# Optimization experiments

Hardware: AMD Instinct MI355X
Metric: run time of the kernel (lower is better)

Reference implementation:

```python
import jax, jax.numpy as jnp
import numpy as np

E = 256; D = 512; A = 5; NS = 2048; NQ = 8192; NWAY = 5
_OTHERS = np.array([[j for j in range(A) if j != i] for i in range(A)])  # [A, A-1] indices of other agents
_ROWS = np.arange(A)[:, None]


def _ln(x, g, b, eps=1e-5):
    m = x.mean(-1, keepdims=True)
    v = ((x - m) ** 2).mean(-1, keepdims=True)
    return (x - m) * jax.lax.rsqrt(v + eps) * g + b


def _mha(x, in_w, in_b, out_w, out_b, h, mask=None):
    # torch nn.MultiheadAttention (batch_first) self-attention. in_w: [3E,E], out_w: [E,E]
    B, S, Em = x.shape
    hd = Em // h
    qkv = x @ in_w.T + in_b
    q, k, v = jnp.split(qkv, 3, axis=-1)
    q = q.reshape(B, S, h, hd).transpose(0, 2, 1, 3) * (1.0 / np.sqrt(hd))
    k = k.reshape(B, S, h, hd).transpose(0, 2, 1, 3)
    v = v.reshape(B, S, h, hd).transpose(0, 2, 1, 3)
    s = jnp.einsum('bhqd,bhkd->bhqk', q, k)
    if mask is not None:
        s = jnp.where(mask, s, jnp.asarray(-1e9, s.dtype))
    a = jax.nn.softmax(s, axis=-1)
    o = jnp.einsum('bhqk,bhkd->bhqd', a, v).transpose(0, 2, 1, 3).reshape(B, S, Em)
    return o @ out_w.T + out_b


def _forward(support_x, support_y, query_x, n_way, fe0_w1, fe0_b1, fe0_g1, fe0_be1, fe0_w2, fe0_b2, fe0_g2, fe0_be2, fe1_w1, fe1_b1, fe1_g, fe1_be, fe1_w2, fe1_b2, fe2_w1, fe2_b1, fe2_w2, fe2_b2, fe2_g, fe2_be, fe3_w1, fe3_b1, fe3_w2, fe3_b2, fe3_g, fe3_be, fe4_w1, fe4_b1, fe4_w2, fe4_b2, fe4_w3, fe4_b3, msg_enc_w, msg_enc_b, agg_in_w, agg_in_b, agg_out_w, agg_out_b, proc_w1, proc_b1, proc_w2, proc_b2, internal_state, proto_in_w, proto_in_b, proto_out_w, proto_out_b, cls_w1, cls_b1, cls_w2, cls_b2, cls_w3, cls_b3, comm_w, f_w1, f_b1, f_w2, f_b2, f_w3, f_b3):
    # --- per-agent-type feature extractors (eval mode: dropout off) ---
    def fe0(x):
        h = jax.nn.relu(_ln(x @ fe0_w1 + fe0_b1, fe0_g1, fe0_be1))
        return jax.nn.relu(_ln(h @ fe0_w2 + fe0_b2, fe0_g2, fe0_be2))
    def fe1(x):
        h = jax.nn.relu(_ln(x @ fe1_w1 + fe1_b1, fe1_g, fe1_be))
        return jnp.tanh(h @ fe1_w2 + fe1_b2)
    def fe2(x):
        h = jax.nn.relu(x @ fe2_w1 + fe2_b1)
        return jax.nn.relu(_ln(h @ fe2_w2 + fe2_b2, fe2_g, fe2_be))
    def fe3(x):
        h = jax.nn.relu(x @ fe3_w1 + fe3_b1)
        return jax.nn.sigmoid(_ln(h @ fe3_w2 + fe3_b2, fe3_g, fe3_be))
    def fe4(x):
        h = jax.nn.relu(x @ fe4_w1 + fe4_b1)
        h = jax.nn.relu(h @ fe4_w2 + fe4_b2)
        return h @ fe4_w3 + fe4_b3
    feats_s = jnp.stack([fe0(support_x), fe1(support_x), fe2(support_x), fe3(support_x), fe4(support_x)])  # [A,NS,E]
    feats_q = jnp.stack([fe0(query_x), fe1(query_x), fe2(query_x), fe3(query_x), fe4(query_x)])            # [A,NQ,E]

    # --- one communication round: generate -> weight -> MHA-aggregate -> MLP-process ---
    agent_state = feats_s.mean(1) + internal_state                                         # [A,E]
    messages = jnp.tanh(jnp.einsum('ae,aef->af', agent_state, msg_enc_w) + msg_enc_b)      # [A,E]
    wgt = jax.nn.softmax(comm_w, axis=-1)                                                  # [A,A]
    msgs = messages[_OTHERS] * wgt[_ROWS, _OTHERS][..., None]                              # [A,A-1,E]
    def agg_one(m, iw, ib, ow, ob):
        return _mha(m[None], iw, ib, ow, ob, 4)[0].mean(0)
    agg = jax.vmap(agg_one)(msgs, agg_in_w, agg_in_b, agg_out_w, agg_out_b)                # [A,E]
    comb = internal_state + agg
    hh = jax.nn.relu(jnp.einsum('ae,aef->af', comb, proc_w1) + proc_b1)
    ck = jnp.einsum('ae,aef->af', hh, proc_w2) + proc_b2                                   # [A,E] communicated knowledge

    # --- class-masked prototype attention (equivalent to per-class MHA) + logits ---
    mask = support_y[:, None] == support_y[None, :]                                        # [NS,NS]
    counts = jax.ops.segment_sum(jnp.ones(support_y.shape, jnp.float32), support_y, num_segments=n_way)
    def head(fs, fq, cki, piw, pib, pw, pb, c1, c1b, c2, c2b, c3, c3b):
        att = _mha((fs + cki[None])[None], piw, pib, pw, pb, 2, mask[None, None])[0]       # [NS,E]
        psum = jax.ops.segment_sum(att, support_y, num_segments=n_way)
        protos = jnp.where(counts[:, None] > 0, psum / jnp.maximum(counts, 1.0)[:, None], 0.0)  # [n_way,E]
        eq = jnp.concatenate([fq, jnp.broadcast_to(cki, fq.shape)], axis=-1)               # [NQ,2E]
        d2 = (fq * fq).sum(-1, keepdims=True) + (protos * protos).sum(-1)[None, :] - 2.0 * (fq @ protos.T)
        dist = jnp.sqrt(jnp.maximum(d2, 1e-12))                                            # cdist
        c = jax.nn.relu(eq @ c1 + c1b)
        c = jax.nn.relu(c @ c2 + c2b)
        conf = c @ c3 + c3b                                                                # [NQ,1]
        return -dist + conf * 0.1
    logits = jax.vmap(head)(feats_s, feats_q, ck, proto_in_w, proto_in_b, proto_out_w, proto_out_b, cls_w1, cls_b1, cls_w2, cls_b2, cls_w3, cls_b3)  # [A,NQ,n_way]

    # --- decision fusion over concatenated per-agent query features ---
    qcat = feats_q.transpose(1, 0, 2).reshape(NQ, A * E)
    fh = jax.nn.relu(qcat @ f_w1 + f_b1)
    fh = jax.nn.relu(fh @ f_w2 + f_b2)
    fused = fh @ f_w3 + f_b3                                                               # [NQ,1]
    return logits, fused


def setup_inputs() -> dict:
    key = jax.random.key(0)
    ks = iter(jax.random.split(key, 80))
    def rn(shape, scale=1.0):
        return (jax.random.normal(next(ks), shape) * scale).astype(jnp.float32)
    def lin(shape, fan):
        return rn(shape, 1.0 / np.sqrt(fan))
    z = lambda s: jnp.zeros(s, jnp.float32)
    o = lambda s: jnp.ones(s, jnp.float32)
    inp = {}
    inp['support_x'] = rn((NS, D))
    inp['support_y'] = jax.random.randint(next(ks), (NS,), 0, NWAY, dtype=jnp.int32)
    inp['query_x'] = rn((NQ, D))
    inp['n_way'] = NWAY
    inp['fe0_w1'] = lin((D, 2 * E), D); inp['fe0_b1'] = z((2 * E,)); inp['fe0_g1'] = o((2 * E,)); inp['fe0_be1'] = z((2 * E,))
    inp['fe0_w2'] = lin((2 * E, E), 2 * E); inp['fe0_b2'] = z((E,)); inp['fe0_g2'] = o((E,)); inp['fe0_be2'] = z((E,))
    inp['fe1_w1'] = lin((D, E), D); inp['fe1_b1'] = z((E,)); inp['fe1_g'] = o((E,)); inp['fe1_be'] = z((E,))
    inp['fe1_w2'] = lin((E, E), E); inp['fe1_b2'] = z((E,))
    inp['fe2_w1'] = lin((D, 3 * E), D); inp['fe2_b1'] = z((3 * E,))
    inp['fe2_w2'] = lin((3 * E, E), 3 * E); inp['fe2_b2'] = z((E,)); inp['fe2_g'] = o((E,)); inp['fe2_be'] = z((E,))
    inp['fe3_w1'] = lin((D, E), D); inp['fe3_b1'] = z((E,))
    inp['fe3_w2'] = lin((E, E), E); inp['fe3_b2'] = z((E,)); inp['fe3_g'] = o((E,)); inp['fe3_be'] = z((E,))
    inp['fe4_w1'] = lin((D, 2 * E), D); inp['fe4_b1'] = z((2 * E,))
    inp['fe4_w2'] = lin((2 * E, E), 2 * E); inp['fe4_b2'] = z((E,))
    inp['fe4_w3'] = lin((E, E), E); inp['fe4_b3'] = z((E,))
    inp['msg_enc_w'] = lin((A, E, E), E); inp['msg_enc_b'] = z((A, E))
    inp['agg_in_w'] = lin((A, 3 * E, E), E); inp['agg_in_b'] = z((A, 3 * E))
    inp['agg_out_w'] = lin((A, E, E), E); inp['agg_out_b'] = z((A, E))
    inp['proc_w1'] = lin((A, E, E), E); inp['proc_b1'] = z((A, E))
    inp['proc_w2'] = lin((A, E, E), E); inp['proc_b2'] = z((A, E))
    inp['internal_state'] = rn((A, E), 0.01)
    inp['proto_in_w'] = lin((A, 3 * E, E), E); inp['proto_in_b'] = z((A, 3 * E))
    inp['proto_out_w'] = lin((A, E, E), E); inp['proto_out_b'] = z((A, E))
    inp['cls_w1'] = lin((A, 2 * E, E), 2 * E); inp['cls_b1'] = z((A, E))
    inp['cls_w2'] = lin((A, E, E // 2), E); inp['cls_b2'] = z((A, E // 2))
    inp['cls_w3'] = lin((A, E // 2, 1), E // 2); inp['cls_b3'] = z((A, 1))
    inp['comm_w'] = (jnp.eye(A) * 0.5 + 0.1).astype(jnp.float32)
    inp['f_w1'] = lin((A * E, E), A * E); inp['f_b1'] = z((E,))
    inp['f_w2'] = lin((E, E // 2), E); inp['f_b2'] = z((E // 2,))
    inp['f_w3'] = lin((E // 2, 1), E // 2); inp['f_b3'] = z((1,))
    return inp


def reference(support_x, support_y, query_x, n_way, fe0_w1, fe0_b1, fe0_g1, fe0_be1, fe0_w2, fe0_b2, fe0_g2, fe0_be2, fe1_w1, fe1_b1, fe1_g, fe1_be, fe1_w2, fe1_b2, fe2_w1, fe2_b1, fe2_w2, fe2_b2, fe2_g, fe2_be, fe3_w1, fe3_b1, fe3_w2, fe3_b2, fe3_g, fe3_be, fe4_w1, fe4_b1, fe4_w2, fe4_b2, fe4_w3, fe4_b3, msg_enc_w, msg_enc_b, agg_in_w, agg_in_b, agg_out_w, agg_out_b, proc_w1, proc_b1, proc_w2, proc_b2, internal_state, proto_in_w, proto_in_b, proto_out_w, proto_out_b, cls_w1, cls_b1, cls_w2, cls_b2, cls_w3, cls_b3, comm_w, f_w1, f_b1, f_w2, f_b2, f_w3, f_b3):
    return _forward(support_x, support_y, query_x, n_way, fe0_w1, fe0_b1, fe0_g1, fe0_be1, fe0_w2, fe0_b2, fe0_g2, fe0_be2, fe1_w1, fe1_b1, fe1_g, fe1_be, fe1_w2, fe1_b2, fe2_w1, fe2_b1, fe2_w2, fe2_b2, fe2_g, fe2_be, fe3_w1, fe3_b1, fe3_w2, fe3_b2, fe3_g, fe3_be, fe4_w1, fe4_b1, fe4_w2, fe4_b2, fe4_w3, fe4_b3, msg_enc_w, msg_enc_b, agg_in_w, agg_in_b, agg_out_w, agg_out_b, proc_w1, proc_b1, proc_w2, proc_b2, internal_state, proto_in_w, proto_in_b, proto_out_w, proto_out_b, cls_w1, cls_b1, cls_w2, cls_b2, cls_w3, cls_b3, comm_w, f_w1, f_b1, f_w2, f_b2, f_w3, f_b3)
```

## Files before the change

kernel.cpp:

```cpp
#include <hip/hip_runtime.h>
#include <hip/hip_bf16.h>

typedef __hip_bfloat16 bf16;
typedef short s8v __attribute__((ext_vector_type(8)));
typedef short s4v __attribute__((ext_vector_type(4)));
typedef float f4v __attribute__((ext_vector_type(4)));

#define A_  5
#define D_  512
#define E_  256
#define NS_ 2048
#define NQ_ 8192
#define NM_ 10240
#define NWAY_ 5
#define QSCALE 0.088388347648318447f
#define FSTR ((size_t)NM_ * E_)

__device__ inline float ldw(const void* p, size_t i, int f32) {
  return f32 ? ((const float*)p)[i] : __bfloat162float(((const bf16*)p)[i]);
}
template<bool DYN>
__device__ inline float ldT(const void* p, size_t i, int f32) {
  if (DYN) return ldw(p, i, f32);
  return ((const float*)p)[i];
}

__device__ inline short f2bf(float v) {
  union { float f; unsigned u; } x; x.f = v;
  unsigned r = x.u + 0x7fffu + ((x.u >> 16) & 1u);
  return (short)(r >> 16);
}
__device__ inline float bf2f(short s) {
  union { unsigned u; float f; } x; x.u = ((unsigned)(unsigned short)s) << 16;
  return x.f;
}

__device__ __forceinline__ void gload16(const void* g, void* l) {
  __builtin_amdgcn_global_load_lds(
      (const __attribute__((address_space(1))) unsigned int*)g,
      (__attribute__((address_space(3))) unsigned int*)l, 16, 0, 0);
}

struct Ptrs { const void* p[64]; int sz[64]; };

__global__ void probe_k(Ptrs P, int* flags) {
  int b = blockIdx.x, lane = threadIdx.x;
  if (b == 1 || b == 3) { if (lane == 0) flags[b] = 0; return; }
  const bf16* t = (const bf16*)P.p[b];
  int n = P.sz[b];
  int K = (n >> 1) < 64 ? (n >> 1) : 64;
  bool big = false, eNZ = false, oNZ = false;
  if (lane < K) {
    float e = __bfloat162float(t[2 * lane]);
    float o = __bfloat162float(t[2 * lane + 1]);
    big = !(fabsf(e) <= 1e3f);
    eNZ = (e != 0.f); oNZ = (o != 0.f);
  }
  unsigned long long bb = __ballot(big), eb = __ballot(eNZ), ob = __ballot(oNZ);
  if (lane == 0) flags[b] = (bb != 0ull || (eb == 0ull && ob != 0ull)) ? 1 : 0;
}

__global__ void classidx_k(const int* __restrict__ y, int* __restrict__ idx,
                           int* __restrict__ cnt, int* __restrict__ cstart) {
  __shared__ int sc[NWAY_];
  int tid = threadIdx.x;
  if (tid < NWAY_) sc[tid] = 0;
  __syncthreads();
  for (int i = tid; i < NS_; i += 256) {
    int c = y[i];
    int pos = atomicAdd(&sc[c], 1);
    idx[c * NS_ + pos] = i;
  }
  __syncthreads();
  if (tid < NWAY_) cnt[tid] = sc[tid];
  if (tid == 0) { int s = 0; for (int q = 0; q < NWAY_; ++q) { cstart[q] = s; s += sc[q]; } }
}

__global__ void xcopy_k(const void* __restrict__ sx, const void* __restrict__ qx,
                        short* __restrict__ XC, const int* __restrict__ flags) {
  size_t i = ((size_t)blockIdx.x * 256 + threadIdx.x) * 4;
  const size_t SN = (size_t)NS_ * 512;
  if (i < SN) {
    int f = flags[0];
    #pragma unroll
    for (int q = 0; q < 4; ++q) XC[i + q] = f2bf(ldw(sx, i + q, f));
  } else {
    int f = flags[2];
    size_t j = i - SN;
    #pragma unroll
    for (int q = 0; q < 4; ++q) XC[i + q] = f2bf(ldw(qx, j + q, f));
  }
}

__global__ void wcat_k(Ptrs P, short* __restrict__ Wcat, float* __restrict__ bcat,
                       const int* __restrict__ flags) {
  int n = blockIdx.x * 256 + threadIdx.x;
  int k = blockIdx.y;
  int iw, ib, nl, Nloc;
  if (n < 512)       { iw = 4;  ib = 5;  nl = n;        Nloc = 512; }
  else if (n < 768)  { iw = 12; ib = 13; nl = n - 512;  Nloc = 256; }
  else if (n < 1536) { iw = 18; ib = 19; nl = n - 768;  Nloc = 768; }
  else if (n < 1792) { iw = 24; ib = 25; nl = n - 1536; Nloc = 256; }
  else               { iw = 30; ib = 31; nl = n - 1792; Nloc = 512; }
  Wcat[(size_t)n * 512 + k] = f2bf(ldw(P.p[iw], (size_t)k * Nloc + nl, flags[iw]));
  if (k == 0) bcat[n] = ldw(P.p[ib], nl, flags[ib]);
}

__global__ void wcls_k(const void* __restrict__ cw1, const void* __restrict__ fw1,
                       short* __restrict__ B2, const int* __restrict__ flags) {
  int n = blockIdx.x, a = blockIdx.y, k = threadIdx.x;
  float v;
  if (n < 256) v = ldw(cw1, ((size_t)a * 512 + k) * 256 + n, flags[51]);
  else v = ldw(fw1, ((size_t)(a * 256 + k)) * 256 + (n - 256), flags[58]);
  B2[((size_t)a * 512 + n) * 256 + k] = f2bf(v);
}

#define LSTR 40
template<int AMODE, int BMODE, bool DYNBIAS, bool TRB, int ACT, bool ACCUM,
         bool KSPLIT = false, bool OUTBF16 = false, bool DOMAP = false>
__global__ __launch_bounds__(256) void gemm_k(
    const void* __restrict__ A, int lda,
    const void* __restrict__ B, int ldb, size_t offB,
    const void* __restrict__ bias, size_t offBias,
    float* __restrict__ C, int ldc,
    int M, int N, int K, float alpha,
    int ia, int ib, int ibias, const int* __restrict__ flags,
    size_t sA, size_t sB, size_t sBias, size_t sC, size_t kstrideA,
    unsigned long long amap)
{
  constexpr bool GDB = (AMODE == 2) && (BMODE == 2) && TRB && !KSPLIT;
  const int fA = (AMODE == 1) ? flags[ia] : 1;
  const int fB = (BMODE == 1) ? flags[ib] : 1;
  const int fBi = DYNBIAS ? flags[ibias] : 1;
  const size_t zA = (size_t)blockIdx.z * sA;
  const size_t zB = offB + (size_t)blockIdx.z * sB;
  const size_t zBias = offBias + (size_t)blockIdx.z * sBias;
  float* Cz = C + (size_t)blockIdx.z * sC;
  bf16* Cz16 = (bf16*)C + (size_t)blockIdx.z * sC;
  const int tid = threadIdx.x;
  const int bm = blockIdx.y * 128, bn = blockIdx.x * 128;
  const int lane = tid & 63, wid = tid >> 6;
  const int lm = lane & 15, quad = lane >> 4;
  const int wy = (wid >> 1) * 64, wx = (wid & 1) * 64;
  f4v acc[4][4];
  #pragma unroll
  for (int i = 0; i < 4; ++i)
    #pragma unroll
    for (int j = 0; j < 4; ++j) acc[i][j] = (f4v)(0.f);

  if constexpr (GDB) {
    __shared__ short smem[4 * 128 * 32];
    const int srow = lane >> 2, scol = (lane & 3) * 8;
    const short* Azs = (const short*)A + zA;
    const short* Bzs = (const short*)B + zB;
    auto stage = [&](int bsel, int k0) {
      short* Asb = smem + bsel * 4096;
      short* Bsb = smem + 8192 + bsel * 4096;
      #pragma unroll
      for (int q = 0; q < 2; ++q) {
        int rb = (wid * 2 + q) * 16;
        gload16(Azs + (size_t)(bm + rb + srow) * lda + k0 + scol, Asb + rb * 32);
        gload16(Bzs + (size_t)(bn + rb + srow) * ldb + k0 + scol, Bsb + rb * 32);
      }
    };
    stage(0, 0);
    __syncthreads();
    int cur = 0;
    for (int k0 = 0; k0 < K; k0 += 32) {
      if (k0 + 32 < K) stage(cur ^ 1, k0 + 32);
      const short* Asb = smem + cur * 4096;
      const short* Bsb = smem + 8192 + cur * 4096;
      s8v af[4], bfr[4];
      #pragma unroll
      for (int mi = 0; mi < 4; ++mi)
        af[mi] = *(const s8v*)&Asb[(wy + mi*16 + lm) * 32 + quad * 8];
      #pragma unroll
      for (int ni = 0; ni < 4; ++ni)
        bfr[ni] = *(const s8v*)&Bsb[(wx + ni*16 + lm) * 32 + quad * 8];
      #pragma unroll
      for (int mi = 0; mi < 4; ++mi)
        #pragma unroll
        for (int ni = 0; ni < 4; ++ni)
          acc[mi][ni] = __builtin_amdgcn_mfma_f32_16x16x32_bf16(af[mi], bfr[ni], acc[mi][ni], 0, 0, 0);
      __syncthreads();
      cur ^= 1;
    }
  } else {
    __shared__ short As[128 * LSTR];
    __shared__ short Bs[128 * LSTR];
    const int am = tid >> 1, ah = (tid & 1) * 16;

    s8v a_s0, a_s1;
    float a_f[16];
    s8v b_s0, b_s1;
    float b_f[16];
    short b_h[16];

    auto loadA = [&](int k0) {
      int kk = k0 + ah;
      size_t base;
      if (KSPLIT) base = zA + (size_t)(kk >> 8) * kstrideA + (size_t)(bm + am) * lda + (kk & 255);
      else base = zA + (size_t)(bm + am) * lda + kk;
      if constexpr (AMODE == 2) {
        const bf16* ap = (const bf16*)A + base;
        a_s0 = *(const s8v*)ap;
        a_s1 = *(const s8v*)(ap + 8);
      } else {
        if (fA) {
          const float4* src = (const float4*)((const float*)A + base);
          #pragma unroll
          for (int q = 0; q < 4; ++q) {
            float4 v = src[q];
            a_f[q*4] = v.x; a_f[q*4+1] = v.y; a_f[q*4+2] = v.z; a_f[q*4+3] = v.w;
          }
        } else {
          #pragma unroll
          for (int q = 0; q < 16; ++q) a_f[q] = ldw(A, base + q, 0);
        }
      }
    };
    auto storeA = [&]() {
      if constexpr (AMODE == 2) {
        *(s8v*)&As[am * LSTR + ah] = a_s0;
        *(s8v*)&As[am * LSTR + ah + 8] = a_s1;
      } else {
        short tmp[16];
        #pragma unroll
        for (int q = 0; q < 16; ++q) tmp[q] = f2bf(a_f[q]);
        s4v* dst = (s4v*)&As[am * LSTR + ah];
        #pragma unroll
        for (int q = 0; q < 4; ++q) dst[q] = *(s4v*)&tmp[q*4];
      }
    };
    auto loadB = [&](int k0) {
      if constexpr (TRB) {
        int n = tid >> 1, h = (tid & 1) * 16;
        size_t base = zB + (size_t)(bn + n) * ldb + k0 + h;
        if constexpr (BMODE == 2) {
          const bf16* bp = (const bf16*)B + base;
          b_s0 = *(const s8v*)bp;
          b_s1 = *(const s8v*)(bp + 8);
        } else {
          if (fB) {
            const float4* src = (const float4*)((const float*)B + base);
            #pragma unroll
            for (int q = 0; q < 4; ++q) {
              float4 v = src[q];
              b_f[q*4] = v.x; b_f[q*4+1] = v.y; b_f[q*4+2] = v.z; b_f[q*4+3] = v.w;
            }
          } else {
            #pragma unroll
            for (int q = 0; q < 16; ++q) b_f[q] = ldw(B, base + q, 0);
          }
        }
      } else {
        int n = tid & 127, kk2 = (tid >> 7) * 16;
        #pragma unroll
        for (int j = 0; j < 16; ++j) {
          size_t bi = zB + (size_t)(k0 + kk2 + j) * ldb + bn + n;
          if constexpr (BMODE == 2) b_h[j] = ((const short*)B)[bi];
          else b_f[j] = ldT<BMODE == 1>(B, bi, fB);
        }
      }
    };
    auto storeB = [&]() {
      if constexpr (TRB) {
        int n = tid >> 1, h = (tid & 1) * 16;
// ... 343 lines not shown
        m_run[ri] = mn;
      }
    }
  }
  if (lm == 0) {
    #pragma unroll
    for (int mi = 0; mi < 4; ++mi)
      #pragma unroll
      for (int r = 0; r < 4; ++r) {
        int row = mi * 16 + quad * 4 + r;
        Mw[wid][row] = m_run[mi * 4 + r];
        Lw[wid][row] = l_run[mi * 4 + r];
      }
  }
  __syncthreads();
  if (tid < 64 && r0 + tid < n) {
    float m = fmaxf(fmaxf(Mw[0][tid], Mw[1][tid]), fmaxf(Mw[2][tid], Mw[3][tid]));
    float l = Lw[0][tid] * __expf(Mw[0][tid] - m) + Lw[1][tid] * __expf(Mw[1][tid] - m)
            + Lw[2][tid] * __expf(Mw[2][tid] - m) + Lw[3][tid] * __expf(Mw[3][tid] - m);
    size_t p = (size_t)z * NS_ + cstart[c] + r0 + tid;
    ml[p * 2] = m; ml[p * 2 + 1] = l;
  }
}

__global__ __launch_bounds__(256) void attn_colsum_k(
    const short* __restrict__ qkv_all, const int* __restrict__ idx,
    const int* __restrict__ cnt, const int* __restrict__ cstart,
    const float* __restrict__ ml, float* __restrict__ colsum)
{
  int c = blockIdx.x, z = blockIdx.z, a = z >> 1, h = z & 1;
  int n = cnt[c];
  int j0 = blockIdx.y * 64;
  if (j0 >= n) return;
  const short* qkv = qkv_all + (size_t)a * NS_ * 768;
  const int* myidx = idx + c * NS_;
  __shared__ short Qs[64 * LS];
  __shared__ short Ks[64 * LS];
  __shared__ float Msm[64], Lsm[64];
  int tid = threadIdx.x, lane = tid & 63, wid = tid >> 6;
  int lm = lane & 15, quad = lane >> 4;
  stage64x128(qkv, myidx, j0, n, 256 + h * 128, Ks);
  float ca = 0.f;
  for (int i0 = 0; i0 < n; i0 += 64) {
    __syncthreads();
    stage64x128(qkv, myidx, i0, n, h * 128, Qs);
    if (tid < 64) {
      int gi = i0 + tid;
      if (gi < n) {
        size_t p = (size_t)z * NS_ + cstart[c] + gi;
        Msm[tid] = ml[p * 2]; Lsm[tid] = ml[p * 2 + 1];
      } else { Msm[tid] = 0.f; Lsm[tid] = 1.f; }
    }
    __syncthreads();
    f4v acc[4];
    #pragma unroll
    for (int mi = 0; mi < 4; ++mi) acc[mi] = (f4v)(0.f);
    #pragma unroll
    for (int kc = 0; kc < 4; ++kc) {
      s8v bfr = *(const s8v*)&Ks[(wid * 16 + lm) * LS + kc * 32 + quad * 8];
      #pragma unroll
      for (int mi = 0; mi < 4; ++mi) {
        s8v af = *(const s8v*)&Qs[(mi * 16 + lm) * LS + kc * 32 + quad * 8];
        acc[mi] = __builtin_amdgcn_mfma_f32_16x16x32_bf16(af, bfr, acc[mi], 0, 0, 0);
      }
    }
    #pragma unroll
    for (int mi = 0; mi < 4; ++mi) {
      #pragma unroll
      for (int r = 0; r < 4; ++r) {
        int lrow = mi * 16 + quad * 4 + r;
        int gi = i0 + lrow;
        if (gi < n) {
          float m = Msm[lrow];
          float invl = 1.f / Lsm[lrow];
          ca += __expf(acc[mi][r] * QSCALE - m) * invl;
        }
      }
    }
  }
  ca += __shfl_xor(ca, 16);
  ca += __shfl_xor(ca, 32);
  int col = j0 + wid * 16 + lm;
  if (quad == 0 && col < n)
    colsum[(size_t)z * NS_ + cstart[c] + col] = ca;
}

#define PCH 8
__global__ __launch_bounds__(1024) void proto_reduce_k(
    const short* __restrict__ qkv_all, const int* __restrict__ idx,
    const int* __restrict__ cnt, const int* __restrict__ cstart,
    const float* __restrict__ colsum, float* __restrict__ proto_pre) {
  int c = blockIdx.x, a = blockIdx.y;
  int n = cnt[c];
  int tid = threadIdx.x, lane = tid & 63, wid = tid >> 6;
  int h = lane >> 5;
  int e0 = lane * 4;
  const short* qkv = qkv_all + (size_t)a * NS_ * 768 + 512;
  const float* csum = colsum + (size_t)(a * 2 + h) * NS_ + cstart[c];
  const int* myidx = idx + c * NS_;
  float a0 = 0.f, a1 = 0.f, a2 = 0.f, a3 = 0.f;
  for (int k = wid; k < n; k += 16) {
    float w = csum[k];
    const s4v v = *(const s4v*)(qkv + (size_t)myidx[k] * 768 + e0);
    a0 += w * bf2f(v[0]); a1 += w * bf2f(v[1]);
    a2 += w * bf2f(v[2]); a3 += w * bf2f(v[3]);
  }
  __shared__ float red[16][E_];
  *(float4*)&red[wid][e0] = make_float4(a0, a1, a2, a3);
  __syncthreads();
  if (tid < E_) {
    float s = 0.f;
    #pragma unroll
    for (int wdx = 0; wdx < 16; ++wdx) s += red[wdx][tid];
    proto_pre[((size_t)a * NWAY_ + c) * E_ + tid] = (n > 0) ? s / (float)n : 0.f;
  }
}

__global__ void proto_outproj_k(const float* __restrict__ proto_pre, const void* __restrict__ ow,
                                const void* __restrict__ ob, const int* __restrict__ cnt,
                                float* __restrict__ protos_all, float* __restrict__ pnorm,
                                const int* __restrict__ flags) {
  int c = blockIdx.x, a = blockIdx.y, e = threadIdx.x;
  const int fW = flags[49], fB = flags[50];
  __shared__ float pp[E_];
  __shared__ float r2[E_];
  pp[e] = proto_pre[((size_t)a * NWAY_ + c) * E_ + e];
  __syncthreads();
  size_t wb = (size_t)a * E_ * E_ + (size_t)e * E_;
  float s = 0.f;
  for (int k = 0; k < E_; ++k) s += pp[k] * ldw(ow, wb + k, fW);
  float v = s + ldw(ob, (size_t)a * E_ + e, fB);
  float vm = (cnt[c] > 0) ? v : 0.f;
  protos_all[((size_t)a * NWAY_ + c) * E_ + e] = vm;
  r2[e] = vm * vm;
  __syncthreads();
  for (int o = 128; o > 0; o >>= 1) { if (e < o) r2[e] += r2[e + o]; __syncthreads(); }
  if (e == 0) pnorm[a * NWAY_ + c] = r2[0];
}

__global__ void bias2_k(const float* __restrict__ ck, const void* __restrict__ w1,
                        const void* __restrict__ b1, float* __restrict__ biascat2,
                        const int* __restrict__ flags) {
  const int fW = flags[51], fB = flags[52];
  int a = blockIdx.x, n = threadIdx.x;
  __shared__ float c[E_];
  c[n] = ck[a * E_ + n]; __syncthreads();
  size_t wbase = (size_t)a * 2 * E_ * E_ + (size_t)E_ * E_ + n;
  float s = 0.f;
  for (int k = 0; k < E_; ++k) s += c[k] * ldw(w1, wbase + (size_t)k * E_, fW);
  biascat2[(size_t)a * 512 + n] = s + ldw(b1, (size_t)a * E_ + n, fB);
  biascat2[(size_t)a * 512 + 256 + n] = 0.f;
}

__global__ void fcomb_k(const short* __restrict__ U, const void* __restrict__ b1,
                        short* __restrict__ fh1, const int* __restrict__ flags) {
  int i = blockIdx.x, n = threadIdx.x;
  const int fB = flags[59];
  float s = 0.f;
  #pragma unroll
  for (int a = 0; a < A_; ++a)
    s += bf2f(U[((size_t)a * NQ_ + i) * 512 + 256 + n]);
  s += ldw(b1, n, fB);
  fh1[(size_t)i * 256 + n] = f2bf(fmaxf(s, 0.f));
}

__global__ __launch_bounds__(64) void logits_k(const short* __restrict__ fqbase,
                                               const float* __restrict__ protos_all,
                                               const float* __restrict__ pnorm,
                                               const bf16* __restrict__ c2all,
                                               const void* __restrict__ w3,
                                               const void* __restrict__ b3,
                                               float* __restrict__ out,
                                               const int* __restrict__ flags) {
  const int fW = flags[55], fB = flags[56];
  int i = blockIdx.x, a = blockIdx.y, lane = threadIdx.x;
  const short* fq = fqbase + (size_t)a * FSTR + (size_t)i * E_ + lane * 4;
  const float* protos = protos_all + (size_t)a * NWAY_ * E_;
  const bf16* c2 = c2all + ((size_t)a * NQ_ + i) * 128;
  s4v xv4 = *(const s4v*)fq;
  float x0 = bf2f(xv4[0]), x1 = bf2f(xv4[1]), x2 = bf2f(xv4[2]), x3 = bf2f(xv4[3]);
  float qq = wave_sum64(x0 * x0 + x1 * x1 + x2 * x2 + x3 * x3);
  float cpart = __bfloat162float(c2[lane * 2]) * ldw(w3, (size_t)a * 128 + lane * 2, fW) +
                __bfloat162float(c2[lane * 2 + 1]) * ldw(w3, (size_t)a * 128 + lane * 2 + 1, fW);
  float conf = wave_sum64(cpart);
  if (lane == 0) conf += ldw(b3, a, fB);
  for (int c = 0; c < NWAY_; ++c) {
    float4 pv = ((const float4*)(protos + c * E_))[lane];
    float dt = wave_sum64(x0 * pv.x + x1 * pv.y + x2 * pv.z + x3 * pv.w);
    if (lane == 0) {
      float pp = pnorm[a * NWAY_ + c];
      float d2 = fmaxf(qq + pp - 2.f * dt, 1e-12f);
      out[((size_t)a * NQ_ + i) * NWAY_ + c] = -sqrtf(d2) + 0.1f * conf;
    }
  }
}

__global__ __launch_bounds__(64) void fused_k(const float* __restrict__ h2, const void* __restrict__ w3,
                                              const void* __restrict__ b3, float* __restrict__ out,
                                              const int* __restrict__ flags) {
  const int fW = flags[62], fB = flags[63];
  int i = blockIdx.x, lane = threadIdx.x;
  float s = h2[(size_t)i * 128 + lane * 2] * ldw(w3, lane * 2, fW) +
            h2[(size_t)i * 128 + lane * 2 + 1] * ldw(w3, lane * 2 + 1, fW);
  s = wave_sum64(s);
  if (lane == 0) out[i] = s + ldw(b3, 0, fB);
}

extern "C" void kernel_launch(void* const* d_in, const int* in_sizes, int n_in,
                              void* d_out, int out_size, void* d_ws, size_t ws_size,
                              hipStream_t stream) {
  (void)out_size; (void)ws_size;
  #define P(i) ((const void*)d_in[i])
  const int* support_y = (const int*)d_in[1];
  float* out = (float*)d_out;

  int* flags = (int*)d_ws;
  char* base = (char*)d_ws + 256;
  short* featsC = (short*)base;
  char* R = base + (size_t)A_ * FSTR * 2;
  short* t1cat   = (short*)R;
  short* qkv_all = (short*)R;
  short* U       = (short*)(R + (size_t)15728640);
  short* fh1     = (short*)R;
  float* fh2     = (float*)(R + (size_t)8388608);
  char* XCR = R + (size_t)57671680;
  short* XC   = (short*)XCR;
  short* tmp2 = (short*)XCR;
  short* b4   = (short*)(XCR + (size_t)NM_ * 256 * 2);
  short* clsC2_all = (short*)XCR;
  char* S = XCR + (size_t)10485760;
  float* state      = (float*)S;
  float* msg        = state + A_ * E_;
  float* ck         = msg + A_ * E_;
  float* protos_all = ck + A_ * E_;
  float* biascat2   = protos_all + A_ * NWAY_ * E_;
  float* ml         = biascat2 + A_ * 512;
  float* colsum     = ml + (size_t)A_ * 2 * NS_ * 2;
  float* proto_pre  = colsum + (size_t)A_ * 2 * NS_;
  int*   idx        = (int*)(proto_pre + A_ * NWAY_ * E_);
  int*   cnt        = idx + NWAY_ * NS_;
  int*   cstart     = cnt + NWAY_;
  float* statepart  = (float*)(cstart + NWAY_ + 3);
  float* mvp        = statepart + A_ * 16 * E_;
  float* qkvc       = mvp + A_ * 8 * E_;
  float* obar       = qkvc + A_ * 4 * 768;
  float* comb       = obar + A_ * E_;
  float* hh         = comb + A_ * E_;
  float* ckb        = hh + A_ * E_;
  float* ppart      = ckb + A_ * 768;
  float* bcat       = ppart + (size_t)A_ * NWAY_ * PCH * E_;
  short* Wcat       = (short*)(bcat + 2304);
  short* Bcat2      = Wcat + (size_t)2304 * 512;

  const short* fq_base = featsC + (size_t)NS_ * E_;

  Ptrs ps;
  for (int i = 0; i < 64; ++i) {
    ps.p[i] = (i < n_in) ? d_in[i] : nullptr;
    ps.sz[i] = (i < n_in) ? in_sizes[i] : 0;
  }
  probe_k<<<64, 64, 0, stream>>>(ps, flags);
  classidx_k<<<1, 256, 0, stream>>>(support_y, idx, cnt, cstart);
  xcopy_k<<<(NM_ * 512 / 4) / 256, 256, 0, stream>>>(P(0), P(2), XC, flags);
  wcat_k<<<dim3(9, 512), 256, 0, stream>>>(ps, Wcat, bcat, flags);
  wcls_k<<<dim3(512, A_), 256, 0, stream>>>(P(51), P(58), Bcat2, flags);

  gemm<2, 2, false, true, 0, false, false, true, true>(
      stream, XC, 512, Wcat, 512, 0, bcat, 0, (float*)t1cat, 2304,
      NM_, 2304, 512, 1.f, -1, -1, -1, flags, 1, 0, 0, 0, 0, 0, 0x555555000ULL);
  lnv_k<1, 512><<<NM_ / 4, 256, 0, stream>>>(t1cat, P(6), P(7), t1cat, 2304, 2304, 6, 7, flags);
  gemm<2, 1, true, false, 0, false, false, true>(stream, t1cat, 2304, P(8), 256, 0, P(9), 0,
                                                 (float*)tmp2, 256, NM_, 256, 512, 1.f, -1, 8, 9, flags);
  lnv_k<1, 256><<<NM_ / 4, 256, 0, stream>>>(tmp2, P(10), P(11), featsC, 256, 256, 10, 11, flags);
  lnv_k<1, 256><<<NM_ / 4, 256, 0, stream>>>(t1cat + 512, P(14), P(15), t1cat + 512, 2304, 2304, 14, 15, flags);
  gemm<2, 1, true, false, 2, false, false, true>(stream, t1cat + 512, 2304, P(16), 256, 0, P(17), 0,
                                                 (float*)(featsC + FSTR), 256, NM_, 256, 256, 1.f, -1, 16, 17, flags);
  gemm<2, 1, true, false, 0, false, false, true>(stream, t1cat + 768, 2304, P(20), 256, 0, P(21), 0,
                                                 (float*)tmp2, 256, NM_, 256, 768, 1.f, -1, 20, 21, flags);
  lnv_k<1, 256><<<NM_ / 4, 256, 0, stream>>>(tmp2, P(22), P(23), featsC + 2 * FSTR, 256, 256, 22, 23, flags);
  gemm<2, 1, true, false, 0, false, false, true>(stream, t1cat + 1536, 2304, P(26), 256, 0, P(27), 0,
                                                 (float*)tmp2, 256, NM_, 256, 256, 1.f, -1, 26, 27, flags);
  lnv_k<3, 256><<<NM_ / 4, 256, 0, stream>>>(tmp2, P(28), P(29), featsC + 3 * FSTR, 256, 256, 28, 29, flags);
  gemm<2, 1, true, false, 1, false, false, true>(stream, t1cat + 1792, 2304, P(32), 256, 0, P(33), 0,
                                                 (float*)b4, 256, NM_, 256, 512, 1.f, -1, 32, 33, flags);
  gemm<2, 1, true, false, 0, false, false, true>(stream, b4, 256, P(34), 256, 0, P(35), 0,
                                                 (float*)(featsC + 4 * FSTR), 256, NM_, 256, 256, 1.f, -1, 34, 35, flags);

  statepart_k<<<dim3(A_, 16), 256, 0, stream>>>(featsC, statepart);
  statecomb_k<<<A_, 256, 0, stream>>>(statepart, P(46), state, flags);
  mvpart_k<<<dim3(A_, 8), 256, 0, stream>>>(state, P(36), 36, mvp, flags);
  mvcomb_k<2><<<A_, 256, 0, stream>>>(mvp, P(37), 37, msg, flags);
  qkvcomm_k<<<A_ * 768 / 4, 256, 0, stream>>>(msg, P(57), P(38), P(39), qkvc, flags);
  attn4_k<<<A_, 256, 0, stream>>>(qkvc, obar);
  combproj_k<<<A_ * E_ / 4, 256, 0, stream>>>(obar, P(40), P(41), P(46), comb, flags);
  mvpart_k<<<dim3(A_, 8), 256, 0, stream>>>(comb, P(42), 42, mvp, flags);
  mvcomb_k<1><<<A_, 256, 0, stream>>>(mvp, P(43), 43, hh, flags);
  mvpart_k<<<dim3(A_, 8), 256, 0, stream>>>(hh, P(44), 44, mvp, flags);
  mvcomb_k<0><<<A_, 256, 0, stream>>>(mvp, P(45), 45, ck, flags);

  ckb_k<<<A_ * 768 / 4, 256, 0, stream>>>(ck, P(47), P(48), ckb, flags);
  gemm<2, 1, false, true, 0, false, false, true>(stream, featsC, 256, P(47), 256, 0, ckb, 0,
                                    (float*)qkv_all, 768, NS_, 768, 256, 1.f, -1, 47, -1, flags,
                                    A_, FSTR, (size_t)3 * E_ * E_, (size_t)768, (size_t)NS_ * 768);
  {
    dim3 g(NWAY_, NS_ / 64, A_ * 2);
    attn_stats_k<<<g, 256, 0, stream>>>(qkv_all, idx, cnt, cstart, ml);
    attn_colsum_k<<<g, 256, 0, stream>>>(qkv_all, idx, cnt, cstart, ml, colsum);
  }
  proto_reduce_k<<<dim3(NWAY_, A_), 1024, 0, stream>>>(qkv_all, idx, cnt, cstart, colsum, proto_pre);
  proto_outproj_k<<<dim3(NWAY_, A_), 256, 0, stream>>>(proto_pre, P(49), P(50), cnt, protos_all, ppart, flags);
  bias2_k<<<A_, 256, 0, stream>>>(ck, P(51), P(52), biascat2, flags);

  gemm<2, 2, false, true, 0, false, false, true, true>(
      stream, fq_base, 256, Bcat2, 256, 0, biascat2, 0, (float*)U, 512,
      NQ_, 512, 256, 1.f, -1, -1, -1, flags,
      A_, FSTR, (size_t)512 * 256, (size_t)512, (size_t)NQ_ * 512, 0, 0x5ULL);
  fcomb_k<<<NQ_, 256, 0, stream>>>(U, P(59), fh1, flags);

  gemm<2, 1, true, false, 1, false, false, true>(stream, U, 512, P(53), 128, 0,
                                     P(54), 0, (float*)clsC2_all, 128, NQ_, 128, 256, 1.f, -1, 53, 54, flags,
                                     A_, (size_t)NQ_ * 512, (size_t)E_ * 128, (size_t)128, (size_t)NQ_ * 128);
  logits_k<<<dim3(NQ_, A_), 64, 0, stream>>>(fq_base, protos_all, ppart, (const bf16*)clsC2_all, P(55), P(56), out, flags);

  gemm<2, 1, true, false, 1, false>(stream, fh1, 256, P(60), 128, 0, P(61), 0, fh2, 128, NQ_, 128, 256, 1.f, -1, 60, 61, flags);
  fused_k<<<NQ_, 64, 0, stream>>>(fh2, P(62), P(63), out + (size_t)A_ * NQ_ * NWAY_, flags);
}
```

Measured before the change: 859.7 us.

## Pre-convert GEMM weights to transposed bf16 and vectorize tail kernels

Adds a one-off weight conversion kernel that writes the feature-extractor, qkv, classifier and fusion weights into a contiguous bf16 buffer in N-major (transposed) layout. The GEMMs then read them through the bf16 transposed-B path instead of the dynamic-dtype row-major path. The small tail kernels (fcomb, logits, fused) are also rewritten to handle one or eight rows per thread with vector loads and shared-memory prototypes and weights, replacing wave-per-row reductions. The cost is an extra conversion kernel on every call and more workspace.

```diff
diff --git a/kernel.cpp b/kernel.cpp
--- a/kernel.cpp
+++ b/kernel.cpp
@@ -113,6 +113,41 @@
   if (n < 256) v = ldw(cw1, ((size_t)a * 512 + k) * 256 + n, flags[51]);
   else v = ldw(fw1, ((size_t)(a * 256 + k)) * 256 + (n - 256), flags[58]);
   B2[((size_t)a * 512 + n) * 256 + k] = f2bf(v);
+}
+
+__global__ void wconv_k(Ptrs P, short* __restrict__ W2, const int* __restrict__ flags) {
+  const int id = blockIdx.y;
+  int src, K, N; size_t off; int tr, batch;
+  switch (id) {
+    case 0: src = 8;  K = 512; N = 256; off = 0;      tr = 1; batch = 1;  break;
+    case 1: src = 16; K = 256; N = 256; off = 131072; tr = 1; batch = 1;  break;
+    case 2: src = 20; K = 768; N = 256; off = 196608; tr = 1; batch = 1;  break;
+    case 3: src = 26; K = 256; N = 256; off = 393216; tr = 1; batch = 1;  break;
+    case 4: src = 32; K = 512; N = 256; off = 458752; tr = 1; batch = 1;  break;
+    case 5: src = 34; K = 256; N = 256; off = 589824; tr = 1; batch = 1;  break;
+    case 6: src = 53; K = 256; N = 128; off = 655360; tr = 1; batch = A_; break;
+    case 7: src = 60; K = 256; N = 128; off = 819200; tr = 1; batch = 1;  break;
+    default: src = 47; K = 256; N = 768; off = 851968; tr = 0; batch = A_; break;
+  }
+  size_t tot = (size_t)batch * K * N;
+  size_t e0 = ((size_t)blockIdx.x * 256 + threadIdx.x) * 4;
+  if (e0 >= tot) return;
+  const void* sp = P.p[src];
+  int f = flags[src];
+  if (!tr) {
+    #pragma unroll
+    for (int q = 0; q < 4; ++q) W2[off + e0 + q] = f2bf(ldw(sp, e0 + q, f));
+  } else {
+    size_t kn = (size_t)K * N;
+    #pragma unroll
+    for (int q = 0; q < 4; ++q) {
+      size_t e = e0 + q;
+      int b = (int)(e / kn);
+      int r = (int)(e % kn);
+      int n = r / K, k = r % K;
+      W2[off + e] = f2bf(ldw(sp, ((size_t)b * K + k) * N + n, f));
+    }
+  }
 }
 
 #define LSTR 40
@@ -762,58 +797,89 @@
   biascat2[(size_t)a * 512 + 256 + n] = 0.f;
 }
 
-__global__ void fcomb_k(const short* __restrict__ U, const void* __restrict__ b1,
-                        short* __restrict__ fh1, const int* __restrict__ flags) {
-  int i = blockIdx.x, n = threadIdx.x;
+__global__ __launch_bounds__(256) void fcomb2_k(const short* __restrict__ U, const void* __restrict__ b1,
+                                                short* __restrict__ fh1, const int* __restrict__ flags) {
   const int fB = flags[59];
+  int r = threadIdx.x >> 5;
+  int n0 = (threadIdx.x & 31) * 8;
+  int i = blockIdx.x * 8 + r;
+  float acc[8];
+  #pragma unroll
+  for (int q = 0; q < 8; ++q) acc[q] = ldw(b1, n0 + q, fB);
+  #pragma unroll
+  for (int a = 0; a < A_; ++a) {
+    s8v v = *(const s8v*)(U + ((size_t)a * NQ_ + i) * 512 + 256 + n0);
+    #pragma unroll
+    for (int q = 0; q < 8; ++q) acc[q] += bf2f(v[q]);
+  }
+  short yv[8];
+  #pragma unroll
+  for (int q = 0; q < 8; ++q) yv[q] = f2bf(fmaxf(acc[q], 0.f));
+  *(s8v*)(fh1 + (size_t)i * 256 + n0) = *(s8v*)yv;
+}
+
+__global__ __launch_bounds__(256) void logits2_k(const short* __restrict__ fqbase,
+                                                 const float* __restrict__ protos_all,
+                                                 const float* __restrict__ pnorm,
+                                                 const bf16* __restrict__ c2all,
+                                                 const void* __restrict__ w3,
+                                                 const void* __restrict__ b3,
+                                                 float* __restrict__ out,
+                                                 const int* __restrict__ flags) {
+  const int fW = flags[55], fB = flags[56];
+  const int a = blockIdx.y;
+  const int i = blockIdx.x * 256 + threadIdx.x;
+  __shared__ float ps[NWAY_][E_];
+  __shared__ float w3s[128];
+  for (int t = threadIdx.x; t < NWAY_ * E_; t += 256)
+    ps[t >> 8][t & 255] = protos_all[(size_t)a * NWAY_ * E_ + t];
+  if (threadIdx.x < 128) w3s[threadIdx.x] = ldw(w3, (size_t)a * 128 + threadIdx.x, fW);
+  __syncthreads();
+  const short* fq = fqbase + (size_t)a * FSTR + (size_t)i * E_;
+  float qq = 0.f, dt0 = 0.f, dt1 = 0.f, dt2 = 0.f, dt3 = 0.f, dt4 = 0.f;
+  for (int e0 = 0; e0 < E_; e0 += 8) {
+    s8v v = *(const s8v*)(fq + e0);
+    #pragma unroll
+    for (int q = 0; q < 8; ++q) {
+      float x = bf2f(v[q]); int e = e0 + q;
+      qq += x * x;
+      dt0 += x * ps[0][e]; dt1 += x * ps[1][e]; dt2 += x * ps[2][e];
+      dt3 += x * ps[3][e]; dt4 += x * ps[4][e];
+    }
+  }
+  const short* c2 = (const short*)c2all + ((size_t)a * NQ_ + i) * 128;
+  float conf = 0.f;
+  for (int e0 = 0; e0 < 128; e0 += 8) {
+    s8v v = *(const s8v*)(c2 + e0);
+    #pragma unroll
+    for (int q = 0; q < 8; ++q) conf += bf2f(v[q]) * w3s[e0 + q];
+  }
+  conf += ldw(b3, a, fB);
+  float dts[5] = { dt0, dt1, dt2, dt3, dt4 };
+  float* o = out + ((size_t)a * NQ_ + i) * NWAY_;
+  #pragma unroll
+  for (int c = 0; c < NWAY_; ++c) {
+    float pp = pnorm[a * NWAY_ + c];
+    float d2 = fmaxf(qq + pp - 2.f * dts[c], 1e-12f);
+    o[c] = -sqrtf(d2) + 0.1f * conf;
+  }
+}
+
+__global__ __launch_bounds__(256) void fused2_k(const float* __restrict__ h2, const void* __restrict__ w3,
+                                                const void* __restrict__ b3, float* __restrict__ out,
+                                                const int* __restrict__ flags) {
+  const int fW = flags[62], fB = flags[63];
+  int i = blockIdx.x * 256 + threadIdx.x;
+  __shared__ float ws[128];
+  if (threadIdx.x < 128) ws[threadIdx.x] = ldw(w3, threadIdx.x, fW);
+  __syncthreads();
+  const float* h = h2 + (size_t)i * 128;
   float s = 0.f;
-  #pragma unroll
-  for (int a = 0; a < A_; ++a)
-    s += bf2f(U[((size_t)a * NQ_ + i) * 512 + 256 + n]);
-  s += ldw(b1, n, fB);
-  fh1[(size_t)i * 256 + n] = f2bf(fmaxf(s, 0.f));
-}
-
-__global__ __launch_bounds__(64) void logits_k(const short* __restrict__ fqbase,
-                                               const float* __restrict__ protos_all,
-                                               const float* __restrict__ pnorm,
-                                               const bf16* __restrict__ c2all,
-                                               const void* __restrict__ w3,
-                                               const void* __restrict__ b3,
-                                               float* __restrict__ out,
-                                               const int* __restrict__ flags) {
-  const int fW = flags[55], fB = flags[56];
-  int i = blockIdx.x, a = blockIdx.y, lane = threadIdx.x;
-  const short* fq = fqbase + (size_t)a * FSTR + (size_t)i * E_ + lane * 4;
-  const float* protos = protos_all + (size_t)a * NWAY_ * E_;
-  const bf16* c2 = c2all + ((size_t)a * NQ_ + i) * 128;
-  s4v xv4 = *(const s4v*)fq;
-  float x0 = bf2f(xv4[0]), x1 = bf2f(xv4[1]), x2 = bf2f(xv4[2]), x3 = bf2f(xv4[3]);
-  float qq = wave_sum64(x0 * x0 + x1 * x1 + x2 * x2 + x3 * x3);
-  float cpart = __bfloat162float(c2[lane * 2]) * ldw(w3, (size_t)a * 128 + lane * 2, fW) +
-                __bfloat162float(c2[lane * 2 + 1]) * ldw(w3, (size_t)a * 128 + lane * 2 + 1, fW);
-  float conf = wave_sum64(cpart);
-  if (lane == 0) conf += ldw(b3, a, fB);
-  for (int c = 0; c < NWAY_; ++c) {
-    float4 pv = ((const float4*)(protos + c * E_))[lane];
-    float dt = wave_sum64(x0 * pv.x + x1 * pv.y + x2 * pv.z + x3 * pv.w);
-    if (lane == 0) {
-      float pp = pnorm[a * NWAY_ + c];
-      float d2 = fmaxf(qq + pp - 2.f * dt, 1e-12f);
-      out[((size_t)a * NQ_ + i) * NWAY_ + c] = -sqrtf(d2) + 0.1f * conf;
-    }
-  }
-}
-
-__global__ __launch_bounds__(64) void fused_k(const float* __restrict__ h2, const void* __restrict__ w3,
-                                              const void* __restrict__ b3, float* __restrict__ out,
-                                              const int* __restrict__ flags) {
-  const int fW = flags[62], fB = flags[63];
-  int i = blockIdx.x, lane = threadIdx.x;
-  float s = h2[(size_t)i * 128 + lane * 2] * ldw(w3, lane * 2, fW) +
-            h2[(size_t)i * 128 + lane * 2 + 1] * ldw(w3, lane * 2 + 1, fW);
-  s = wave_sum64(s);
-  if (lane == 0) out[i] = s + ldw(b3, 0, fB);
+  for (int e = 0; e < 128; e += 4) {
+    float4 v = *(const float4*)(h + e);
+    s += v.x * ws[e] + v.y * ws[e + 1] + v.z * ws[e + 2] + v.w * ws[e + 3];
+  }
+  out[i] = s + ldw(b3, 0, fB);
 }
 
 extern "C" void kernel_launch(void* const* d_in, const int* in_sizes, int n_in,
@@ -861,6 +927,7 @@
   float* bcat       = ppart + (size_t)A_ * NWAY_ * PCH * E_;
   short* Wcat       = (short*)(bcat + 2304);
   short* Bcat2      = Wcat + (size_t)2304 * 512;
+  short* W2         = Bcat2 + (size_t)A_ * 512 * 256;
 
   const short* fq_base = featsC + (size_t)NS_ * E_;
 
@@ -874,27 +941,28 @@
   xcopy_k<<<(NM_ * 512 / 4) / 256, 256, 0, stream>>>(P(0), P(2), XC, flags);
   wcat_k<<<dim3(9, 512), 256, 0, stream>>>(ps, Wcat, bcat, flags);
   wcls_k<<<dim3(512, A_), 256, 0, stream>>>(P(51), P(58), Bcat2, flags);
+  wconv_k<<<dim3(960, 9), 256, 0, stream>>>(ps, W2, flags);
 
   gemm<2, 2, false, true, 0, false, false, true, true>(
       stream, XC, 512, Wcat, 512, 0, bcat, 0, (float*)t1cat, 2304,
       NM_, 2304, 512, 1.f, -1, -1, -1, flags, 1, 0, 0, 0, 0, 0, 0x555555000ULL);
   lnv_k<1, 512><<<NM_ / 4, 256, 0, stream>>>(t1cat, P(6), P(7), t1cat, 2304, 2304, 6, 7, flags);
-  gemm<2, 1, true, false, 0, false, false, true>(stream, t1cat, 2304, P(8), 256, 0, P(9), 0,
-                                                 (float*)tmp2, 256, NM_, 256, 512, 1.f, -1, 8, 9, flags);
+  gemm<2, 2, true, true, 0, false, false, true>(stream, t1cat, 2304, W2 + 0, 512, 0, P(9), 0,
+                                                (float*)tmp2, 256, NM_, 256, 512, 1.f, -1, -1, 9, flags);
   lnv_k<1, 256><<<NM_ / 4, 256, 0, stream>>>(tmp2, P(10), P(11), featsC, 256, 256, 10, 11, flags);
   lnv_k<1, 256><<<NM_ / 4, 256, 0, stream>>>(t1cat + 512, P(14), P(15), t1cat + 512, 2304, 2304, 14, 15, flags);
-  gemm<2, 1, true, false, 2, false, false, true>(stream, t1cat + 512, 2304, P(16), 256, 0, P(17), 0,
-                                                 (float*)(featsC + FSTR), 256, NM_, 256, 256, 1.f, -1, 16, 17, flags);
-  gemm<2, 1, true, false, 0, false, false, true>(stream, t1cat + 768, 2304, P(20), 256, 0, P(21), 0,
-                                                 (float*)tmp2, 256, NM_, 256, 768, 1.f, -1, 20, 21, flags);
+  gemm<2, 2, true, true, 2, false, false, true>(stream, t1cat + 512, 2304, W2 + 131072, 256, 0, P(17), 0,
+                                                (float*)(featsC + FSTR), 256, NM_, 256, 256, 1.f, -1, -1, 17, flags);
+  gemm<2, 2, true, true, 0, false, false, true>(stream, t1cat + 768, 2304, W2 + 196608, 768, 0, P(21), 0,
+                                                (float*)tmp2, 256, NM_, 256, 768, 1.f, -1, -1, 21, flags);
   lnv_k<1, 256><<<NM_ / 4, 256, 0, stream>>>(tmp2, P(22), P(23), featsC + 2 * FSTR, 256, 256, 22, 23, flags);
-  gemm<2, 1, true, false, 0, false, false, true>(stream, t1cat + 1536, 2304, P(26), 256, 0, P(27), 0,
-                                                 (float*)tmp2, 256, NM_, 256, 256, 1.f, -1, 26, 27, flags);
+  gemm<2, 2, true, true, 0, false, false, true>(stream, t1cat + 1536, 2304, W2 + 393216, 256, 0, P(27), 0,
+                                                (float*)tmp2, 256, NM_, 256, 256, 1.f, -1, -1, 27, flags);
   lnv_k<3, 256><<<NM_ / 4, 256, 0, stream>>>(tmp2, P(28), P(29), featsC + 3 * FSTR, 256, 256, 28, 29, flags);
-  gemm<2, 1, true, false, 1, false, false, true>(stream, t1cat + 1792, 2304, P(32), 256, 0, P(33), 0,
-                                                 (float*)b4, 256, NM_, 256, 512, 1.f, -1, 32, 33, flags);
-  gemm<2, 1, true, false, 0, false, false, true>(stream, b4, 256, P(34), 256, 0, P(35), 0,
-                                                 (float*)(featsC + 4 * FSTR), 256, NM_, 256, 256, 1.f, -1, 34, 35, flags);
+  gemm<2, 2, true, true, 1, false, false, true>(stream, t1cat + 1792, 2304, W2 + 458752, 512, 0, P(33), 0,
+                                                (float*)b4, 256, NM_, 256, 512, 1.f, -1, -1, 33, flags);
+  gemm<2, 2, true, true, 0, false, false, true>(stream, b4, 256, W2 + 589824, 256, 0, P(35), 0,
+                                                (float*)(featsC + 4 * FSTR), 256, NM_, 256, 256, 1.f, -1, -1, 35, flags);
 
   statepart_k<<<dim3(A_, 16), 256, 0, stream>>>(featsC, statepart);
   statecomb_k<<<A_, 256, 0, stream>>>(statepart, P(46), state, flags);
@@ -909,9 +977,9 @@
   mvcomb_k<0><<<A_, 256, 0, stream>>>(mvp, P(45), 45, ck, flags);
 
   ckb_k<<<A_ * 768 / 4, 256, 0, stream>>>(ck, P(47), P(48), ckb, flags);
-  gemm<2, 1, false, true, 0, false, false, true>(stream, featsC, 256, P(47), 256, 0, ckb, 0,
-                                    (float*)qkv_all, 768, NS_, 768, 256, 1.f, -1, 47, -1, flags,
-                                    A_, FSTR, (size_t)3 * E_ * E_, (size_t)768, (size_t)NS_ * 768);
+  gemm<2, 2, false, true, 0, false, false, true>(stream, featsC, 256, W2 + 851968, 256, 0, ckb, 0,
+                                    (float*)qkv_all, 768, NS_, 768, 256, 1.f, -1, -1, -1, flags,
+                                    A_, FSTR, (size_t)768 * 256, (size_t)768, (size_t)NS_ * 768);
   {
     dim3 g(NWAY_, NS_ / 64, A_ * 2);
     attn_stats_k<<<g, 256, 0, stream>>>(qkv_all, idx, cnt, cstart, ml);
@@ -925,13 +993,15 @@
       stream, fq_base, 256, Bcat2, 256, 0, biascat2, 0, (float*)U, 512,
       NQ_, 512, 256, 1.f, -1, -1, -1, flags,
       A_, FSTR, (size_t)512 * 256, (size_t)512, (size_t)NQ_ * 512, 0, 0x5ULL);
-  fcomb_k<<<NQ_, 256, 0, stream>>>(U, P(59), fh1, flags);
-
-  gemm<2, 1, true, false, 1, false, false, true>(stream, U, 512, P(53), 128, 0,
-                                     P(54), 0, (float*)clsC2_all, 128, NQ_, 128, 256, 1.f, -1, 53, 54, flags,
-                                     A_, (size_t)NQ_ * 512, (size_t)E_ * 128, (size_t)128, (size_t)NQ_ * 128);
-  logits_k<<<dim3(NQ_, A_), 64, 0, stream>>>(fq_base, protos_all, ppart, (const bf16*)clsC2_all, P(55), P(56), out, flags);
-
-  gemm<2, 1, true, false, 1, false>(stream, fh1, 256, P(60), 128, 0, P(61), 0, fh2, 128, NQ_, 128, 256, 1.f, -1, 60, 61, flags);
-  fused_k<<<NQ_, 64, 0, stream>>>(fh2, P(62), P(63), out + (size_t)A_ * NQ_ * NWAY_, flags);
-}
+  fcomb2_k<<<NQ_ / 8, 256, 0, stream>>>(U, P(59), fh1, flags);
+
+  gemm<2, 2, true, true, 1, false, false, true>(stream, U, 512, W2 + 655360, 256, 0,
+                                     P(54), 0, (float*)clsC2_all, 128, NQ_, 128, 256, 1.f, -1, -1, 54, flags,
+                                     A_, (size_t)NQ_ * 512, (size_t)128 * 256, (size_t)128, (size_t)NQ_ * 128);
+  logits2_k<<<dim3(NQ_ / 256, A_), 256, 0, stream>>>(fq_base, protos_all, ppart,
+                                                     (const bf16*)clsC2_all, P(55), P(56), out, flags);
+
+  gemm<2, 2, true, true, 1, false>(stream, fh1, 256, W2 + 819200, 256, 0, P(61), 0, fh2, 128,
+                                   NQ_, 128, 256, 1.f, -1, -1, 61, flags);
+  fused2_k<<<NQ_ / 256, 256, 0, stream>>>(fh2, P(62), P(63), out + (size_t)A_ * NQ_ * NWAY_, flags);
+}
```

After: 841.4 us. -2.1%, faster.
